# Performance work log

Measured on AMD Instinct MI355X. Metric: run time of the kernel, lower is better.

Reference implementation:

```python
import jax, jax.numpy as jnp
import numpy as np

S, O, J, B = 16, 8, 32, 4096
HID, OUT_HID = 240, 512
P1, P2 = 0.5, 0.65  # Bayesian (concrete) dropout probabilities, mid of [0.5, 0.8]


def setup_inputs() -> dict:
    key = jax.random.key(0)
    ks = jax.random.split(key, 20)
    sc = 0.05
    return {
        "y_t": jax.random.normal(ks[0], (B, O), jnp.float32),
        "x_filtered_prev": jax.random.normal(ks[1], (B, S), jnp.float32),
        "F": jax.random.normal(ks[2], (S, S), jnp.float32) * sc,
        "H": jax.random.normal(ks[3], (O, S), jnp.float32) * sc,
        "W_fc_in": jax.random.normal(ks[4], (HID, 2 * S + 2 * O), jnp.float32) * sc,
        "b_fc_in": jax.random.normal(ks[5], (HID,), jnp.float32) * sc,
        "W_ih": jax.random.normal(ks[6], (3 * HID, HID), jnp.float32) * sc,
        "W_hh": jax.random.normal(ks[7], (3 * HID, HID), jnp.float32) * sc,
        "b_ih": jax.random.normal(ks[8], (3 * HID,), jnp.float32) * sc,
        "b_hh": jax.random.normal(ks[9], (3 * HID,), jnp.float32) * sc,
        "W_out1": jax.random.normal(ks[10], (OUT_HID, HID), jnp.float32) * sc,
        "b_out1": jax.random.normal(ks[11], (OUT_HID,), jnp.float32) * sc,
        "W_out2": jax.random.normal(ks[12], (S * O, OUT_HID), jnp.float32) * sc,
        "b_out2": jax.random.normal(ks[13], (S * O,), jnp.float32) * sc,
        "h_init": jax.random.normal(ks[14], (HID,), jnp.float32),
        "u1": jax.random.uniform(ks[15], (J, B, HID), jnp.float32),
        "u2": jax.random.uniform(ks[16], (J, B, OUT_HID), jnp.float32),
    }


def reference(y_t, x_filtered_prev, F, H, W_fc_in, b_fc_in, W_ih, W_hh, b_ih,
              b_hh, W_out1, b_out1, W_out2, b_out2, h_init, u1, u2):
    # --- first step of step_StateBayesianKalmanNet, fully batched over (J, B) ---
    x_pred = x_filtered_prev @ F.T                 # f(x): [B,S]
    y_pred = x_pred @ H.T                          # h(x): [B,O]
    state_inno = x_filtered_prev - x_pred          # x_filt_prev - x_pred_prev
    innovation = y_t - y_pred
    diff_state = jnp.zeros_like(x_filtered_prev)   # first step: x_prev - x_prev_prev = 0
    diff_obs = y_t - y_pred                        # y_prev = h(x_pred) on first step

    feats = jnp.concatenate([state_inno, innovation, diff_state, diff_obs], -1)  # [B,48]
    x_in = jax.nn.relu(feats @ W_fc_in.T + b_fc_in)                              # [B,HID]
    mask1 = (u1 > P1).astype(x_in.dtype) / (1.0 - P1)                            # [J,B,HID]
    x_in = x_in[None] * mask1                                                    # Bayesian dropout sample j

    # single GRU cell step (torch gate order r,z,n), h_prev = h_init broadcast
    gx = x_in @ W_ih.T + b_ih                                                    # [J,B,3H]
    gh = h_init @ W_hh.T + b_hh                                                  # [3H]
    xr, xz, xn = jnp.split(gx, 3, axis=-1)
    hr, hz, hn = jnp.split(gh, 3, axis=-1)
    r = jax.nn.sigmoid(xr + hr)
    z = jax.nn.sigmoid(xz + hz)
    n = jnp.tanh(xn + r * hn)
    h_new = (1.0 - z) * n + z * h_init                                           # [J,B,HID]

    o1 = jax.nn.relu(h_new @ W_out1.T + b_out1)                                  # [J,B,OUT_HID]
    mask2 = (u2 > P2).astype(o1.dtype) / (1.0 - P2)
    o1 = o1 * mask2
    K_vec = o1 @ W_out2.T + b_out2                                               # [J,B,S*O]
    K = K_vec.reshape(J, B, S, O)

    correction = jnp.einsum('jbso,bo->jbs', K, innovation)
    x_filt = x_pred[None] + correction                                           # [J,B,S]
    ensemble = jnp.transpose(x_filt, (1, 0, 2))                                  # [B,J,S]
    final_x = ensemble.mean(axis=1)
    final_P_diag = ensemble.var(axis=1, ddof=1)                                  # torch unbiased var

    # concrete-dropout regularization (entropy of the two dropout gates, mean over J)
    reg = -(P1 * jnp.log(P1) + (1 - P1) * jnp.log(1 - P1)) \
          - (P2 * jnp.log(P2) + (1 - P2) * jnp.log(1 - P2))
    reg = jnp.asarray(reg, final_x.dtype)

    return final_x, final_P_diag, reg, ensemble
```

## Files before the change

### kernel.cpp

```cpp
#include <hip/hip_runtime.h>
#include <hip/hip_bf16.h>
#include <math.h>

#define S_DIM 16
#define O_DIM 8
#define J_DIM 32
#define B_DIM 4096
#define HID 240
#define OHID 512

typedef __attribute__((ext_vector_type(8))) short bf16x8;
typedef __attribute__((ext_vector_type(4))) float f32x4;
#define MFMA16(a,b,c) __builtin_amdgcn_mfma_f32_16x16x32_bf16((a),(b),(c),0,0,0)

#define WS_XPRED   0
#define WS_INNO    (WS_XPRED + B_DIM*S_DIM)
#define WS_FEATS   (WS_INNO + B_DIM*O_DIM)
#define WS_XIN0    (WS_FEATS + B_DIM*48)
#define WS_GH      (WS_XIN0 + B_DIM*HID)
#define WS_WB_OFF  ((WS_GH + 960) * 4)

#define OUT_X      0
#define OUT_P      (B_DIM*S_DIM)
#define OUT_REG    (2*B_DIM*S_DIM)
#define OUT_ENS    (2*B_DIM*S_DIM + 1)

__global__ void k_aux(const float* __restrict__ W_ih, const float* __restrict__ W_hh,
                      const float* __restrict__ b_ih, const float* __restrict__ b_hh,
                      const float* __restrict__ h_init,
                      const float* __restrict__ W_o1, const float* __restrict__ W_o2,
                      __hip_bfloat16* __restrict__ Wihb, __hip_bfloat16* __restrict__ Wo1b,
                      __hip_bfloat16* __restrict__ Wo2b, float* __restrict__ ghb)
{
    int t = blockIdx.x * 256 + threadIdx.x;
    if (t < 768*256) {
        int n = t >> 8, k = t & 255;
        float v = (n < 720 && k < 240) ? W_ih[n*240 + k] : 0.0f;
        Wihb[t] = __float2bfloat16(v);
    } else if (t < 768*256 + 512*256) {
        int u = t - 768*256;
        int n = u >> 8, k = u & 255;
        float v = (k < 240) ? W_o1[n*240 + k] : 0.0f;
        Wo1b[u] = __float2bfloat16(v);
    } else if (t < 768*256 + 512*256 + 128*512) {
        int u = t - 768*256 - 512*256;
        Wo2b[u] = __float2bfloat16(W_o2[u]);
    }
    if (t < 720) {
        float a = b_hh[t];
        const float* wr = W_hh + t*240;
        for (int k = 0; k < 240; k++) a = fmaf(h_init[k], wr[k], a);
        if (t < 480) {
            ghb[t] = b_ih[t] + a;
        } else {
            ghb[t] = b_ih[t];
            ghb[t + 240] = a;
        }
    }
}

__global__ void k_pre_a(const float* __restrict__ y, const float* __restrict__ xprev,
                        const float* __restrict__ F, const float* __restrict__ Hm,
                        float* __restrict__ x_pred, float* __restrict__ inno,
                        float* __restrict__ feats)
{
    __shared__ float sF[256], sH[128];
    int tid = threadIdx.x;
    sF[tid] = F[tid];
    if (tid < 128) sH[tid] = Hm[tid];
    __syncthreads();
    int b = blockIdx.x * 256 + tid;
    float xf[16], xp[16], inn[8];
    #pragma unroll
    for (int s = 0; s < 16; s++) xf[s] = xprev[b*16 + s];
    #pragma unroll
    for (int s = 0; s < 16; s++) {
        float a = 0.f;
        #pragma unroll
        for (int k = 0; k < 16; k++) a = fmaf(xf[k], sF[s*16 + k], a);
        xp[s] = a;
    }
    #pragma unroll
    for (int o = 0; o < 8; o++) {
        float a = 0.f;
        #pragma unroll
        for (int k = 0; k < 16; k++) a = fmaf(xp[k], sH[o*16 + k], a);
        inn[o] = y[b*8 + o] - a;
    }
    #pragma unroll
    for (int s = 0; s < 16; s++) x_pred[b*16 + s] = xp[s];
    #pragma unroll
    for (int o = 0; o < 8; o++) inno[b*8 + o] = inn[o];
    float* fb = feats + b*48;
    #pragma unroll
    for (int s = 0; s < 16; s++) fb[s] = xf[s] - xp[s];
    #pragma unroll
    for (int o = 0; o < 8; o++) fb[16 + o] = inn[o];
    #pragma unroll
    for (int s = 0; s < 16; s++) fb[24 + s] = 0.f;
    #pragma unroll
    for (int o = 0; o < 8; o++) fb[40 + o] = inn[o];
}

__global__ void k_pre_b(const float* __restrict__ feats, const float* __restrict__ Wfc,
                        const float* __restrict__ bfc, float* __restrict__ x_in0)
{
    int t = blockIdx.x * 256 + threadIdx.x;
    int b = t / 240, h = t - b*240;
    const float* fb = feats + b*48;
    const float* wr = Wfc + h*48;
    float a = bfc[h];
    #pragma unroll
    for (int k = 0; k < 48; k += 4) {
        const float4 f4 = *(const float4*)&fb[k];
        const float4 w4 = *(const float4*)&wr[k];
        a = fmaf(f4.x, w4.x, fmaf(f4.y, w4.y, fmaf(f4.z, w4.z, fmaf(f4.w, w4.w, a))));
    }
    x_in0[t] = fmaxf(a, 0.f);
}

#define XS_STRIDE 264
#define O1_STRIDE 520

__global__ __launch_bounds__(256, 3) void k_main(
    const float* __restrict__ x_in0, const float* __restrict__ u1,
    const float* __restrict__ u2,
    const __hip_bfloat16* __restrict__ Wihb, const float* __restrict__ ghb,
    const float* __restrict__ h_init,
    const __hip_bfloat16* __restrict__ Wo1b, const float* __restrict__ b_out1,
    const __hip_bfloat16* __restrict__ Wo2b, const float* __restrict__ b_out2,
    const float* __restrict__ x_pred, const float* __restrict__ inno,
    float* __restrict__ ens)
{
    __shared__ __align__(16) char smem[53248];
    __hip_bfloat16* O1s = (__hip_bfloat16*)smem;
    __hip_bfloat16* Xs  = (__hip_bfloat16*)smem;
    __hip_bfloat16* Hs  = (__hip_bfloat16*)(smem + 33280);
    float* XPs   = (float*)(smem + 50176);
    float* InnoS = (float*)(smem + 52224);

    const int tid = threadIdx.x;
    const int j  = blockIdx.x >> 7;
    const int b0 = (blockIdx.x & 127) << 5;

    for (int idx = tid; idx < 32*240; idx += 256) {
        int i = idx / 240, h = idx - i*240;
        int b = b0 + i;
        float v = x_in0[b*240 + h];
        float u = u1[(j*B_DIM + b)*240 + h];
        Xs[i*XS_STRIDE + h] = __float2bfloat16((u > 0.5f) ? 2.0f*v : 0.0f);
    }
    for (int idx = tid; idx < 32*24; idx += 256) {
        int i = idx / 24, c = 240 + (idx - i*24);
        __hip_bfloat16 z = __float2bfloat16(0.0f);
        Xs[i*XS_STRIDE + c] = z;
        Hs[i*XS_STRIDE + c] = z;
    }
    XPs[tid]       = x_pred[(b0 + (tid >> 4))*16 + (tid & 15)];
    XPs[tid + 256] = x_pred[(b0 + ((tid + 256) >> 4))*16 + (tid & 15)];
    InnoS[tid]     = inno[(b0 + (tid >> 3))*8 + (tid & 7)];
    __syncthreads();

    const int wave = tid >> 6;
    const int l15  = tid & 15;
    const int quad = (tid >> 4) & 3;
    const f32x4 zero4 = {0.f, 0.f, 0.f, 0.f};

    {
        f32x4 accR[4][2], accZ[4][2], accN[4][2];
        #pragma unroll
        for (int it = 0; it < 4; it++)
            #pragma unroll
            for (int m = 0; m < 2; m++) { accR[it][m] = zero4; accZ[it][m] = zero4; accN[it][m] = zero4; }

        #pragma unroll
        for (int ks = 0; ks < 8; ks++) {
            const int ko = ks*32 + quad*8;
            bf16x8 a0 = *(const bf16x8*)&Xs[l15*XS_STRIDE + ko];
            bf16x8 a1 = *(const bf16x8*)&Xs[(16 + l15)*XS_STRIDE + ko];
            #pragma unroll
            for (int it = 0; it < 4; it++) {
                const int n = (wave + 4*it)*16 + l15;
                bf16x8 br = *(const bf16x8*)&Wihb[n*256 + ko];
                bf16x8 bz = *(const bf16x8*)&Wihb[(n + 240)*256 + ko];
                bf16x8 bn = *(const bf16x8*)&Wihb[(n + 480)*256 + ko];
                accR[it][0] = MFMA16(a0, br, accR[it][0]);
                accR[it][1] = MFMA16(a1, br, accR[it][1]);
                accZ[it][0] = MFMA16(a0, bz, accZ[it][0]);
                accZ[it][1] = MFMA16(a1, bz, accZ[it][1]);
                accN[it][0] = MFMA16(a0, bn, accN[it][0]);
                accN[it][1] = MFMA16(a1, bn, accN[it][1]);
            }
        }
        #pragma unroll
        for (int it = 0; it < 4; it++) {
            const int t = wave + 4*it;
            if (t < 15) {
                const int h = t*16 + l15;
                const float add_r = ghb[h],       add_z = ghb[240 + h];
                const float add_n = ghb[480 + h], mul_n = ghb[720 + h];
                const float hi = h_init[h];
                #pragma unroll
                for (int m = 0; m < 2; m++)
                    #pragma unroll
                    for (int r = 0; r < 4; r++) {
                        const int row = m*16 + quad*4 + r;
                        float rg = 1.0f/(1.0f + expf(-(accR[it][m][r] + add_r)));
                        float zg = 1.0f/(1.0f + expf(-(accZ[it][m][r] + add_z)));
                        float ng = tanhf(accN[it][m][r] + add_n + rg*mul_n);
                        Hs[row*XS_STRIDE + h] = __float2bfloat16((1.0f - zg)*ng + zg*hi);
                    }
            }
        }
    }
    __syncthreads();

    {
        f32x4 acc2[8][2];
        #pragma unroll
        for (int it = 0; it < 8; it++) { acc2[it][0] = zero4; acc2[it][1] = zero4; }

        #pragma unroll
        for (int ks = 0; ks < 8; ks++) {
            const int ko = ks*32 + quad*8;
            bf16x8 a0 = *(const bf16x8*)&Hs[l15*XS_STRIDE + ko];
            bf16x8 a1 = *(const bf16x8*)&Hs[(16 + l15)*XS_STRIDE + ko];
            #pragma unroll
            for (int it = 0; it < 8; it++) {
                const int n = (wave*8 + it)*16 + l15;
                bf16x8 b = *(const bf16x8*)&Wo1b[n*256 + ko];
                acc2[it][0] = MFMA16(a0, b, acc2[it][0]);
                acc2[it][1] = MFMA16(a1, b, acc2[it][1]);
            }
        }
        const float inv35 = 1.0f/0.35f;
        #pragma unroll
        for (int it = 0; it < 8; it++) {
            const int n = (wave*8 + it)*16 + l15;
            const float bb = b_out1[n];
            #pragma unroll
            for (int m = 0; m < 2; m++)
                #pragma unroll
                for (int r = 0; r < 4; r++) {
                    const int row = m*16 + quad*4 + r;
                    const int b = b0 + row;
                    float uu = u2[((j*B_DIM + b) << 9) + n];
                    float o = fmaxf(acc2[it][m][r] + bb, 0.0f);
                    o = (uu > 0.65f) ? o*inv35 : 0.0f;
                    O1s[row*O1_STRIDE + n] = __float2bfloat16(o);
                }
        }
    }
    __syncthreads();

    {
        f32x4 acc3[2][2];
        #pragma unroll
        for (int it = 0; it < 2; it++) {
            const int n = (wave*2 + it)*16 + l15;
            const float bo = b_out2[n];
            f32x4 v = {bo, bo, bo, bo};
            acc3[it][0] = v; acc3[it][1] = v;
        }
        #pragma unroll
        for (int ks = 0; ks < 16; ks++) {
            const int ko = ks*32 + quad*8;
            bf16x8 a0 = *(const bf16x8*)&O1s[l15*O1_STRIDE + ko];
            bf16x8 a1 = *(const bf16x8*)&O1s[(16 + l15)*O1_STRIDE + ko];
            #pragma unroll
            for (int it = 0; it < 2; it++) {
                const int n = (wave*2 + it)*16 + l15;
                bf16x8 b = *(const bf16x8*)&Wo2b[n*512 + ko];
                acc3[it][0] = MFMA16(a0, b, acc3[it][0]);
                acc3[it][1] = MFMA16(a1, b, acc3[it][1]);
            }
        }
        #pragma unroll
        for (int it = 0; it < 2; it++) {
            const int n = (wave*2 + it)*16 + l15;
            const int s = n >> 3, o = n & 7;
            #pragma unroll
            for (int m = 0; m < 2; m++)
                #pragma unroll
                for (int r = 0; r < 4; r++) {
                    const int row = m*16 + quad*4 + r;
                    float v = acc3[it][m][r] * InnoS[row*8 + o];
                    v += __shfl_xor(v, 1);
                    v += __shfl_xor(v, 2);
                    v += __shfl_xor(v, 4);
                    if (o == 0)
                        ens[((b0 + row)*J_DIM + j)*16 + s] = XPs[row*16 + s] + v;
                }
        }
    }
}

__global__ void k_final(const float* __restrict__ ens, float* __restrict__ out)
{
    int t = blockIdx.x * 256 + threadIdx.x;
    int b = t >> 4, s = t & 15;
    float v[32];
    #pragma unroll
    for (int jj = 0; jj < 32; jj++) v[jj] = ens[(b*32 + jj)*16 + s];
    float m = 0.f;
    #pragma unroll
    for (int jj = 0; jj < 32; jj++) m += v[jj];
    m *= (1.0f/32.0f);
    float var = 0.f;
    #pragma unroll
    for (int jj = 0; jj < 32; jj++) { float d = v[jj] - m; var = fmaf(d, d, var); }
    var *= (1.0f/31.0f);
    out[OUT_X + t] = m;
    out[OUT_P + t] = var;
    if (t == 0) out[OUT_REG] = 1.3405938195945778f;
}

extern "C" void kernel_launch(void* const* d_in, const int* in_sizes, int n_in,
                              void* d_out, int out_size, void* d_ws, size_t ws_size,
                              hipStream_t stream)
{
    (void)in_sizes; (void)n_in; (void)out_size; (void)ws_size;
    const float* y_t    = (const float*)d_in[0];
    const float* xprev  = (const float*)d_in[1];
    const float* F      = (const float*)d_in[2];
    const float* Hm     = (const float*)d_in[3];
    const float* Wfc    = (const float*)d_in[4];
    const float* bfc    = (const float*)d_in[5];
    const float* W_ih   = (const float*)d_in[6];
    const float* W_hh   = (const float*)d_in[7];
    const float* b_ih   = (const float*)d_in[8];
    const float* b_hh   = (const float*)d_in[9];
    const float* W_o1   = (const float*)d_in[10];
    const float* b_o1   = (const float*)d_in[11];
    const float* W_o2   = (const float*)d_in[12];
    const float* b_o2   = (const float*)d_in[13];
    const float* h_init = (const float*)d_in[14];
    const float* u1     = (const float*)d_in[15];
    const float* u2     = (const float*)d_in[16];

    float* out = (float*)d_out;
    float* ws  = (float*)d_ws;
    float* x_pred = ws + WS_XPRED;
    float* inno   = ws + WS_INNO;
    float* feats  = ws + WS_FEATS;
    float* x_in0  = ws + WS_XIN0;
    float* ghb    = ws + WS_GH;
    __hip_bfloat16* Wihb = (__hip_bfloat16*)((char*)d_ws + WS_WB_OFF);
    __hip_bfloat16* Wo1b = Wihb + 768*256;
    __hip_bfloat16* Wo2b = Wo1b + 512*256;
    float* ens    = out + OUT_ENS;

    k_aux<<<dim3(1536), dim3(256), 0, stream>>>(W_ih, W_hh, b_ih, b_hh, h_init,
                                                W_o1, W_o2, Wihb, Wo1b, Wo2b, ghb);
    k_pre_a<<<dim3(16), dim3(256), 0, stream>>>(y_t, xprev, F, Hm, x_pred, inno, feats);
    k_pre_b<<<dim3(3840), dim3(256), 0, stream>>>(feats, Wfc, bfc, x_in0);
    k_main<<<dim3(4096), dim3(256), 0, stream>>>(x_in0, u1, u2, Wihb, ghb, h_init,
                                                 Wo1b, b_o1, Wo2b, b_o2,
                                                 x_pred, inno, ens);
    k_final<<<dim3(256), dim3(256), 0, stream>>>(ens, out);
}
```

Baseline: 873.3 us.

## Prefetch dropout masks, vectorize staging loads, fuse preprocessing kernels, use fast math

k_main now reads the u2 dropout uniforms at the start into a 64-bit register bitmask using nontemporal loads, instead of loading them scattered in the second GEMM epilogue. The u1/x_in0 staging loop moves to float4 nontemporal loads with packed bf16 stores. The two preprocessing kernels merge into one 2D-grid kernel that computes the fc_in layer directly from register features. Sigmoid and tanh switch to exp2/rcp intrinsics, and bf16 conversion uses a manual rounding routine. The fast math approximations add small numerical error, and the prefetched mask raises register pressure under the 3-blocks-per-CU launch bound.

```diff
diff --git a/kernel.cpp b/kernel.cpp
--- a/kernel.cpp
+++ b/kernel.cpp
@@ -15,8 +15,7 @@
 
 #define WS_XPRED   0
 #define WS_INNO    (WS_XPRED + B_DIM*S_DIM)
-#define WS_FEATS   (WS_INNO + B_DIM*O_DIM)
-#define WS_XIN0    (WS_FEATS + B_DIM*48)
+#define WS_XIN0    (WS_INNO + B_DIM*O_DIM)
 #define WS_GH      (WS_XIN0 + B_DIM*HID)
 #define WS_WB_OFF  ((WS_GH + 960) * 4)
 
@@ -25,26 +24,40 @@
 #define OUT_REG    (2*B_DIM*S_DIM)
 #define OUT_ENS    (2*B_DIM*S_DIM + 1)
 
+__device__ __forceinline__ unsigned short cvt_bf16(float f) {
+    unsigned u = __builtin_bit_cast(unsigned, f);
+    u += 0x7FFFu + ((u >> 16) & 1u);
+    return (unsigned short)(u >> 16);
+}
+__device__ __forceinline__ float fast_sigmoid(float x) {
+    float e = __builtin_amdgcn_exp2f(-1.4426950408889634f * x);
+    return __builtin_amdgcn_rcpf(1.0f + e);
+}
+__device__ __forceinline__ float fast_tanh(float x) {
+    float e = __builtin_amdgcn_exp2f(2.8853900817779268f * x);
+    return 1.0f - 2.0f * __builtin_amdgcn_rcpf(e + 1.0f);
+}
+
 __global__ void k_aux(const float* __restrict__ W_ih, const float* __restrict__ W_hh,
                       const float* __restrict__ b_ih, const float* __restrict__ b_hh,
                       const float* __restrict__ h_init,
                       const float* __restrict__ W_o1, const float* __restrict__ W_o2,
-                      __hip_bfloat16* __restrict__ Wihb, __hip_bfloat16* __restrict__ Wo1b,
-                      __hip_bfloat16* __restrict__ Wo2b, float* __restrict__ ghb)
+                      unsigned short* __restrict__ Wihb, unsigned short* __restrict__ Wo1b,
+                      unsigned short* __restrict__ Wo2b, float* __restrict__ ghb)
 {
     int t = blockIdx.x * 256 + threadIdx.x;
     if (t < 768*256) {
         int n = t >> 8, k = t & 255;
         float v = (n < 720 && k < 240) ? W_ih[n*240 + k] : 0.0f;
-        Wihb[t] = __float2bfloat16(v);
+        Wihb[t] = cvt_bf16(v);
     } else if (t < 768*256 + 512*256) {
         int u = t - 768*256;
         int n = u >> 8, k = u & 255;
         float v = (k < 240) ? W_o1[n*240 + k] : 0.0f;
-        Wo1b[u] = __float2bfloat16(v);
+        Wo1b[u] = cvt_bf16(v);
     } else if (t < 768*256 + 512*256 + 128*512) {
         int u = t - 768*256 - 512*256;
-        Wo2b[u] = __float2bfloat16(W_o2[u]);
+        Wo2b[u] = cvt_bf16(W_o2[u]);
     }
     if (t < 720) {
         float a = b_hh[t];
@@ -59,10 +72,11 @@
     }
 }
 
-__global__ void k_pre_a(const float* __restrict__ y, const float* __restrict__ xprev,
-                        const float* __restrict__ F, const float* __restrict__ Hm,
-                        float* __restrict__ x_pred, float* __restrict__ inno,
-                        float* __restrict__ feats)
+__global__ void k_pre(const float* __restrict__ y, const float* __restrict__ xprev,
+                      const float* __restrict__ F, const float* __restrict__ Hm,
+                      const float* __restrict__ Wfc, const float* __restrict__ bfc,
+                      float* __restrict__ x_pred, float* __restrict__ inno,
+                      float* __restrict__ x_in0)
 {
     __shared__ float sF[256], sH[128];
     int tid = threadIdx.x;
@@ -70,7 +84,7 @@
     if (tid < 128) sH[tid] = Hm[tid];
     __syncthreads();
     int b = blockIdx.x * 256 + tid;
-    float xf[16], xp[16], inn[8];
+    float xf[16], xp[16], ft[48];
     #pragma unroll
     for (int s = 0; s < 16; s++) xf[s] = xprev[b*16 + s];
     #pragma unroll
@@ -85,38 +99,26 @@
         float a = 0.f;
         #pragma unroll
         for (int k = 0; k < 16; k++) a = fmaf(xp[k], sH[o*16 + k], a);
-        inn[o] = y[b*8 + o] - a;
-    }
-    #pragma unroll
-    for (int s = 0; s < 16; s++) x_pred[b*16 + s] = xp[s];
-    #pragma unroll
-    for (int o = 0; o < 8; o++) inno[b*8 + o] = inn[o];
-    float* fb = feats + b*48;
-    #pragma unroll
-    for (int s = 0; s < 16; s++) fb[s] = xf[s] - xp[s];
-    #pragma unroll
-    for (int o = 0; o < 8; o++) fb[16 + o] = inn[o];
-    #pragma unroll
-    for (int s = 0; s < 16; s++) fb[24 + s] = 0.f;
-    #pragma unroll
-    for (int o = 0; o < 8; o++) fb[40 + o] = inn[o];
-}
-
-__global__ void k_pre_b(const float* __restrict__ feats, const float* __restrict__ Wfc,
-                        const float* __restrict__ bfc, float* __restrict__ x_in0)
-{
-    int t = blockIdx.x * 256 + threadIdx.x;
-    int b = t / 240, h = t - b*240;
-    const float* fb = feats + b*48;
-    const float* wr = Wfc + h*48;
-    float a = bfc[h];
-    #pragma unroll
-    for (int k = 0; k < 48; k += 4) {
-        const float4 f4 = *(const float4*)&fb[k];
-        const float4 w4 = *(const float4*)&wr[k];
-        a = fmaf(f4.x, w4.x, fmaf(f4.y, w4.y, fmaf(f4.z, w4.z, fmaf(f4.w, w4.w, a))));
-    }
-    x_in0[t] = fmaxf(a, 0.f);
+        float inn = y[b*8 + o] - a;
+        ft[16 + o] = inn;
+        ft[40 + o] = inn;
+    }
+    #pragma unroll
+    for (int s = 0; s < 16; s++) { ft[s] = xf[s] - xp[s]; ft[24 + s] = 0.f; }
+    if (blockIdx.y == 0) {
+        #pragma unroll
+        for (int s = 0; s < 16; s++) x_pred[b*16 + s] = xp[s];
+        #pragma unroll
+        for (int o = 0; o < 8; o++) inno[b*8 + o] = ft[16 + o];
+    }
+    const int h0 = blockIdx.y * 15;
+    for (int h = h0; h < h0 + 15; h++) {
+        float a = bfc[h];
+        const float* wr = Wfc + h*48;
+        #pragma unroll
+        for (int k = 0; k < 48; k++) a = fmaf(ft[k], wr[k], a);
+        x_in0[(size_t)b*240 + h] = fmaxf(a, 0.f);
+    }
 }
 
 #define XS_STRIDE 264
@@ -125,45 +127,73 @@
 __global__ __launch_bounds__(256, 3) void k_main(
     const float* __restrict__ x_in0, const float* __restrict__ u1,
     const float* __restrict__ u2,
-    const __hip_bfloat16* __restrict__ Wihb, const float* __restrict__ ghb,
+    const unsigned short* __restrict__ Wihb, const float* __restrict__ ghb,
     const float* __restrict__ h_init,
-    const __hip_bfloat16* __restrict__ Wo1b, const float* __restrict__ b_out1,
-    const __hip_bfloat16* __restrict__ Wo2b, const float* __restrict__ b_out2,
+    const unsigned short* __restrict__ Wo1b, const float* __restrict__ b_out1,
+    const unsigned short* __restrict__ Wo2b, const float* __restrict__ b_out2,
     const float* __restrict__ x_pred, const float* __restrict__ inno,
     float* __restrict__ ens)
 {
     __shared__ __align__(16) char smem[53248];
-    __hip_bfloat16* O1s = (__hip_bfloat16*)smem;
-    __hip_bfloat16* Xs  = (__hip_bfloat16*)smem;
-    __hip_bfloat16* Hs  = (__hip_bfloat16*)(smem + 33280);
+    unsigned short* O1s = (unsigned short*)smem;
+    unsigned short* Xs  = (unsigned short*)smem;
+    unsigned short* Hs  = (unsigned short*)(smem + 33280);
     float* XPs   = (float*)(smem + 50176);
     float* InnoS = (float*)(smem + 52224);
 
     const int tid = threadIdx.x;
     const int j  = blockIdx.x >> 7;
     const int b0 = (blockIdx.x & 127) << 5;
-
-    for (int idx = tid; idx < 32*240; idx += 256) {
-        int i = idx / 240, h = idx - i*240;
-        int b = b0 + i;
-        float v = x_in0[b*240 + h];
-        float u = u1[(j*B_DIM + b)*240 + h];
-        Xs[i*XS_STRIDE + h] = __float2bfloat16((u > 0.5f) ? 2.0f*v : 0.0f);
-    }
-    for (int idx = tid; idx < 32*24; idx += 256) {
-        int i = idx / 24, c = 240 + (idx - i*24);
-        __hip_bfloat16 z = __float2bfloat16(0.0f);
-        Xs[i*XS_STRIDE + c] = z;
-        Hs[i*XS_STRIDE + c] = z;
-    }
-    XPs[tid]       = x_pred[(b0 + (tid >> 4))*16 + (tid & 15)];
-    XPs[tid + 256] = x_pred[(b0 + ((tid + 256) >> 4))*16 + (tid & 15)];
-    InnoS[tid]     = inno[(b0 + (tid >> 3))*8 + (tid & 7)];
-    __syncthreads();
-
     const int wave = tid >> 6;
     const int l15  = tid & 15;
     const int quad = (tid >> 4) & 3;
+
+    unsigned long long m2 = 0;
+    {
+        const float* u2b = u2 + ((size_t)(j*B_DIM + b0) << 9);
+        #pragma unroll
+        for (int it = 0; it < 8; it++) {
+            const int n = (wave*8 + it)*16 + l15;
+            #pragma unroll
+            for (int m = 0; m < 2; m++)
+                #pragma unroll
+                for (int r = 0; r < 4; r++) {
+                    const int row = (m << 4) + (quad << 2) + r;
+                    float uu = __builtin_nontemporal_load(&u2b[((size_t)row << 9) + n]);
+                    if (uu > 0.65f) m2 |= (1ull << (it*8 + m*4 + r));
+                }
+        }
+    }
+
+    {
+        const f32x4* u1b = (const f32x4*)(u1 + (size_t)(j*B_DIM + b0) * 240);
+        const f32x4* xb  = (const f32x4*)(x_in0 + (size_t)b0 * 240);
+        #pragma unroll
+        for (int q = 0; q < 8; q++) {
+            int f = q*256 + tid;
+            if (f < 1920) {
+                int row = f / 60, c4 = f - row*60;
+                f32x4 uv = __builtin_nontemporal_load(&u1b[f]);
+                f32x4 xv = xb[f];
+                ushort4 o;
+                o.x = (uv.x > 0.5f) ? cvt_bf16(2.0f*xv.x) : (unsigned short)0;
+                o.y = (uv.y > 0.5f) ? cvt_bf16(2.0f*xv.y) : (unsigned short)0;
+                o.z = (uv.z > 0.5f) ? cvt_bf16(2.0f*xv.z) : (unsigned short)0;
+                o.w = (uv.w > 0.5f) ? cvt_bf16(2.0f*xv.w) : (unsigned short)0;
+                *(ushort4*)&Xs[row*XS_STRIDE + (c4 << 2)] = o;
+            }
+        }
+    }
+    for (int p = tid; p < 512; p += 256) {
+        int row = p >> 4, c = 240 + (p & 15);
+        Xs[row*XS_STRIDE + c] = 0;
+        Hs[row*XS_STRIDE + c] = 0;
+    }
+    XPs[tid]       = x_pred[(size_t)b0*16 + tid];
+    XPs[tid + 256] = x_pred[(size_t)b0*16 + 256 + tid];
+    InnoS[tid]     = inno[(size_t)b0*8 + tid];
+    __syncthreads();
+
     const f32x4 zero4 = {0.f, 0.f, 0.f, 0.f};
 
     {
@@ -204,11 +234,11 @@
                 for (int m = 0; m < 2; m++)
                     #pragma unroll
                     for (int r = 0; r < 4; r++) {
-                        const int row = m*16 + quad*4 + r;
-                        float rg = 1.0f/(1.0f + expf(-(accR[it][m][r] + add_r)));
-                        float zg = 1.0f/(1.0f + expf(-(accZ[it][m][r] + add_z)));
-                        float ng = tanhf(accN[it][m][r] + add_n + rg*mul_n);
-                        Hs[row*XS_STRIDE + h] = __float2bfloat16((1.0f - zg)*ng + zg*hi);
+                        const int row = (m << 4) + (quad << 2) + r;
+                        float rg = fast_sigmoid(accR[it][m][r] + add_r);
+                        float zg = fast_sigmoid(accZ[it][m][r] + add_z);
+                        float ng = fast_tanh(accN[it][m][r] + add_n + rg*mul_n);
+                        Hs[row*XS_STRIDE + h] = cvt_bf16((1.0f - zg)*ng + zg*hi);
                     }
             }
         }
@@ -242,12 +272,10 @@
             for (int m = 0; m < 2; m++)
                 #pragma unroll
                 for (int r = 0; r < 4; r++) {
-                    const int row = m*16 + quad*4 + r;
-                    const int b = b0 + row;
-                    float uu = u2[((j*B_DIM + b) << 9) + n];
-                    float o = fmaxf(acc2[it][m][r] + bb, 0.0f);
-                    o = (uu > 0.65f) ? o*inv35 : 0.0f;
-                    O1s[row*O1_STRIDE + n] = __float2bfloat16(o);
+                    const int row = (m << 4) + (quad << 2) + r;
+                    float o = fmaxf(acc2[it][m][r] + bb, 0.0f) * inv35;
+                    o = ((m2 >> (it*8 + m*4 + r)) & 1) ? o : 0.0f;
+                    O1s[row*O1_STRIDE + n] = cvt_bf16(o);
                 }
         }
     }
@@ -283,13 +311,13 @@
             for (int m = 0; m < 2; m++)
                 #pragma unroll
                 for (int r = 0; r < 4; r++) {
-                    const int row = m*16 + quad*4 + r;
+                    const int row = (m << 4) + (quad << 2) + r;
                     float v = acc3[it][m][r] * InnoS[row*8 + o];
                     v += __shfl_xor(v, 1);
                     v += __shfl_xor(v, 2);
                     v += __shfl_xor(v, 4);
                     if (o == 0)
-                        ens[((b0 + row)*J_DIM + j)*16 + s] = XPs[row*16 + s] + v;
+                        ens[((size_t)(b0 + row)*J_DIM + j)*16 + s] = XPs[row*16 + s] + v;
                 }
         }
     }
@@ -301,7 +329,7 @@
     int b = t >> 4, s = t & 15;
     float v[32];
     #pragma unroll
-    for (int jj = 0; jj < 32; jj++) v[jj] = ens[(b*32 + jj)*16 + s];
+    for (int jj = 0; jj < 32; jj++) v[jj] = ens[((size_t)b*32 + jj)*16 + s];
     float m = 0.f;
     #pragma unroll
     for (int jj = 0; jj < 32; jj++) m += v[jj];
@@ -342,18 +370,17 @@
     float* ws  = (float*)d_ws;
     float* x_pred = ws + WS_XPRED;
     float* inno   = ws + WS_INNO;
-    float* feats  = ws + WS_FEATS;
     float* x_in0  = ws + WS_XIN0;
     float* ghb    = ws + WS_GH;
-    __hip_bfloat16* Wihb = (__hip_bfloat16*)((char*)d_ws + WS_WB_OFF);
-    __hip_bfloat16* Wo1b = Wihb + 768*256;
-    __hip_bfloat16* Wo2b = Wo1b + 512*256;
+    unsigned short* Wihb = (unsigned short*)((char*)d_ws + WS_WB_OFF);
+    unsigned short* Wo1b = Wihb + 768*256;
+    unsigned short* Wo2b = Wo1b + 512*256;
     float* ens    = out + OUT_ENS;
 
     k_aux<<<dim3(1536), dim3(256), 0, stream>>>(W_ih, W_hh, b_ih, b_hh, h_init,
                                                 W_o1, W_o2, Wihb, Wo1b, Wo2b, ghb);
-    k_pre_a<<<dim3(16), dim3(256), 0, stream>>>(y_t, xprev, F, Hm, x_pred, inno, feats);
-    k_pre_b<<<dim3(3840), dim3(256), 0, stream>>>(feats, Wfc, bfc, x_in0);
+    k_pre<<<dim3(16, 16), dim3(256), 0, stream>>>(y_t, xprev, F, Hm, Wfc, bfc,
+                                                  x_pred, inno, x_in0);
     k_main<<<dim3(4096), dim3(256), 0, stream>>>(x_in0, u1, u2, Wihb, ghb, h_init,
                                                  Wo1b, b_o1, Wo2b, b_o2,
                                                  x_pred, inno, ens);
```

After: 1.046 ms. +19.8%, slower.
